# Kernel tuning notes

Measured on AMD Instinct MI355X. Metric: run time of the kernel, lower is better.

## Reference

```python
import jax, jax.numpy as jnp
import numpy as np


def _pair_loss(s, r):
    # s: [N, 4] sampled lidar, r: [M, 4] raw lidar; use xyz only
    a = s[:, :3]
    b = r[:, :3]
    # pairwise Euclidean distances, [N, M] (torch.cdist p=2)
    sq = (jnp.sum(a * a, axis=1)[:, None]
          + jnp.sum(b * b, axis=1)[None, :]
          - 2.0 * (a @ b.T))
    dist = jnp.sqrt(jnp.maximum(sq, 0.0))
    # dist[argmin(dim=0), j] == min over rows; dist[i, argmin(dim=1)] == min over cols
    min_over_sampled = jnp.min(dist, axis=0)  # [M] nearest sampled point per raw point
    min_over_raw = jnp.min(dist, axis=1)      # [N] nearest raw point per sampled point
    LB = jnp.mean(min_over_sampled)
    LF = jnp.mean(min_over_raw)
    LM = jnp.max(min_over_raw)
    return 5.0 * LB + 1.0 * LF + LM


def setup_inputs() -> dict:
    key = jax.random.key(0)
    k1, k2 = jax.random.split(key)
    B, N, M = 2, 4096, 16384
    sampled = jax.random.normal(k1, (B, N, 4), dtype=jnp.float32)
    raw = jax.random.normal(k2, (B, M, 4), dtype=jnp.float32)
    return {"sampled": sampled, "raw": raw}


def reference(sampled, raw):
    # list of pairs == batch dim; loss averaged over pairs
    losses = jax.vmap(_pair_loss)(sampled, raw)  # [B]
    return jnp.mean(losses)
```

## Files before the change

### kernel.cpp

```cpp
#include <hip/hip_runtime.h>
#include <math.h>

constexpr int BB = 2, NN = 4096, MM = 16384;
constexpr int CSL = 4;
constexpr int RSL = 16;
constexpr unsigned INFBITS = 0x7F800000u;
constexpr ushort ONEB = 0x3F80;

typedef __attribute__((ext_vector_type(8)))  short  short8;
typedef __attribute__((ext_vector_type(8)))  ushort ushort8;
typedef __attribute__((ext_vector_type(16))) float  f32x16;

__device__ __forceinline__ ushort f2bf(float f) {
    unsigned u = __float_as_uint(f);
    u += 0x7FFF + ((u >> 16) & 1);
    return (ushort)(u >> 16);
}
__device__ __forceinline__ void split2(float v, ushort& h, ushort& l) {
    h = f2bf(v);
    l = f2bf(v - __uint_as_float(((unsigned)h) << 16));
}
__device__ __forceinline__ float vmin16(const f32x16& c) {
    float a0 = fminf(fminf(c[0], c[1]),   fminf(c[2], c[3]));
    float a1 = fminf(fminf(c[4], c[5]),   fminf(c[6], c[7]));
    float a2 = fminf(fminf(c[8], c[9]),   fminf(c[10], c[11]));
    float a3 = fminf(fminf(c[12], c[13]), fminf(c[14], c[15]));
    return fminf(fminf(a0, a1), fminf(a2, a3));
}

__global__ __launch_bounds__(256) void pack_kernel(
    const float* __restrict__ sampled, const float* __restrict__ raw,
    ushort* __restrict__ As, ushort* __restrict__ Ar,
    unsigned* __restrict__ counter)
{
    const int g = blockIdx.x * 256 + threadIdx.x;
    if (g == 0) *counter = 0u;
    float4 v;
    ushort* dst;
    if (g < BB * NN) {
        v = ((const float4*)sampled)[g];
        dst = As + ((size_t)(g >> 5) << 9) + (g & 31) * 8;
    } else {
        const int p = g - BB * NN;
        v = ((const float4*)raw)[p];
        dst = Ar + ((size_t)(p >> 5) << 9) + (p & 31) * 8;
    }
    float n = fmaf(v.z, v.z, fmaf(v.y, v.y, v.x * v.x));
    ushort hx,lx,hy,ly,hz,lz,hn,ln;
    split2(-2.f * v.x, hx, lx); split2(-2.f * v.y, hy, ly);
    split2(-2.f * v.z, hz, lz); split2(n, hn, ln);
    *(ushort8*)(dst)       = ushort8{hx,hy,hz,hx,hy,hz,lx,ly};
    *(ushort8*)(dst + 256) = ushort8{lz,hn,ln,ONEB,ONEB,0,0,0};
}

__global__ __launch_bounds__(256) void pair_kernel(
    const float* __restrict__ sampled,
    const float* __restrict__ raw,
    const ushort* __restrict__ As, const ushort* __restrict__ Ar,
    float* __restrict__ rowpart,
    float* __restrict__ colpart)
{
    const int gx = blockIdx.x, tid = threadIdx.x;
    const int w = tid >> 6, lane = tid & 63, half = lane >> 5, l31 = lane & 31;
    const float INF = __uint_as_float(INFBITS);
    const f32x16 zero = {0.f,0.f,0.f,0.f,0.f,0.f,0.f,0.f,
                         0.f,0.f,0.f,0.f,0.f,0.f,0.f,0.f};

    int b, base, sl;
    const ushort* Ap;
    float4 v;
    float* outp;
    if (gx < 1024) {
        int idx = gx; b = idx >> 9; idx &= 511;
        const int og = idx >> 2; sl = idx & 3;
        base = og * 128 + w * 32;
        v = ((const float4*)raw)[(size_t)b * MM + base + l31];
        Ap = As + ((size_t)(b * (NN / 32) + sl * 32) << 9) + lane * 8;
        outp = colpart + ((size_t)sl * BB + b) * MM + base;
    } else {
        int idx = gx - 1024; b = idx >> 9; idx &= 511;
        const int og = idx >> 4; sl = idx & 15;
        base = og * 128 + w * 32;
        v = ((const float4*)sampled)[(size_t)b * NN + base + l31];
        Ap = Ar + ((size_t)(b * (MM / 32) + sl * 32) << 9) + lane * 8;
        outp = rowpart + ((size_t)sl * BB + b) * NN + base;
    }

    short8 bfr;
    {
        float n = fmaf(v.z, v.z, fmaf(v.y, v.y, v.x * v.x));
        ushort hx,lx,hy,ly,hz,lz,hn,ln;
        split2(v.x, hx, lx); split2(v.y, hy, ly);
        split2(v.z, hz, lz); split2(n, hn, ln);
        ushort8 w0 = ushort8{hx,hy,hz,lx,ly,lz,hx,hy};
        ushort8 w1 = ushort8{hz,ONEB,ONEB,hn,ln,0,0,0};
        ushort8 sel = half ? w1 : w0;
        bfr = *(short8*)&sel;
    }

    float acc = INF;
#pragma unroll 2
    for (int t = 0; t < 32; ++t) {
        short8 af = *(const short8*)(Ap + ((size_t)t << 9));
        f32x16 c = __builtin_amdgcn_mfma_f32_32x32x16_bf16(af, bfr, zero, 0, 0, 0);
        acc = fminf(acc, vmin16(c));
    }
    acc = fminf(acc, __shfl_xor(acc, 32, 64));
    if (lane < 32) outp[lane] = fmaxf(acc, 0.f);
}

__global__ __launch_bounds__(256) void reduce_kernel(
    const float* __restrict__ rowpart,
    const float* __restrict__ colpart,
    float* __restrict__ part,
    unsigned* __restrict__ counter,
    float* __restrict__ out)
{
    const int k = blockIdx.x, b = k >> 6, s = k & 63;
    const int tid = threadIdx.x;
    const float INF = __uint_as_float(INFBITS);

    const int col = s * 256 + tid;
    float v = INF;
#pragma unroll
    for (int sl = 0; sl < CSL; ++sl)
        v = fminf(v, colpart[((size_t)sl * BB + b) * MM + col]);
    float sB = sqrtf(v);

    const int row = s * 64 + (tid & 63);
    const int jq  = tid >> 6;
    float wv2 = INF;
#pragma unroll
    for (int q = 0; q < RSL / 4; ++q)
        wv2 = fminf(wv2, rowpart[((size_t)(jq * (RSL / 4) + q) * BB + b) * NN + row]);
    __shared__ float rred[4][64];
    rred[jq][tid & 63] = wv2;
    __syncthreads();
    float sF = 0.f, mF = 0.f;
    if (tid < 64) {
        float rmn = fminf(fminf(rred[0][tid], rred[1][tid]),
                          fminf(rred[2][tid], rred[3][tid]));
        float d = sqrtf(rmn);
        sF = d; mF = d;
    }

    for (int m = 1; m < 64; m <<= 1) {
        sB += __shfl_xor(sB, m, 64);
        sF += __shfl_xor(sF, m, 64);
        mF = fmaxf(mF, __shfl_xor(mF, m, 64));
    }
    __shared__ float red[3][4];
    const int lane = tid & 63, wvi = tid >> 6;
    if (lane == 0) { red[0][wvi] = sB; red[1][wvi] = sF; red[2][wvi] = mF; }
    __syncthreads();

    __shared__ bool isLast;
    if (tid == 0) {
        part[k * 3 + 0] = red[0][0] + red[0][1] + red[0][2] + red[0][3];
        part[k * 3 + 1] = red[1][0] + red[1][1] + red[1][2] + red[1][3];
        part[k * 3 + 2] = fmaxf(fmaxf(red[2][0], red[2][1]),
                                fmaxf(red[2][2], red[2][3]));
        __threadfence();
        isLast = (atomicAdd(counter, 1u) == 127u);
    }
    __syncthreads();
    if (!isLast) return;

    __threadfence();
    volatile const float* vp = part;
    float fB = 0.f, fF = 0.f, fM = 0.f;
    if (tid < 128) {
        fB = vp[tid * 3 + 0]; fF = vp[tid * 3 + 1]; fM = vp[tid * 3 + 2];
    }
    for (int m = 1; m < 64; m <<= 1) {
        fB += __shfl_xor(fB, m, 64);
        fF += __shfl_xor(fF, m, 64);
        fM = fmaxf(fM, __shfl_xor(fM, m, 64));
    }
    __shared__ float fin[2][3];
    if (tid < 128 && (tid & 63) == 0) {
        fin[tid >> 6][0] = fB; fin[tid >> 6][1] = fF; fin[tid >> 6][2] = fM;
    }
    __syncthreads();
    if (tid == 0) {
        float l0 = 5.f * fin[0][0] / (float)MM + fin[0][1] / (float)NN + fin[0][2];
        float l1 = 5.f * fin[1][0] / (float)MM + fin[1][1] / (float)NN + fin[1][2];
        *out = 0.5f * (l0 + l1);
    }
}

extern "C" void kernel_launch(void* const* d_in, const int* in_sizes, int n_in,
                              void* d_out, int out_size, void* d_ws, size_t ws_size,
                              hipStream_t stream) {
    const float* sampled = (const float*)d_in[0];
    const float* raw     = (const float*)d_in[1];
    ushort* As     = (ushort*)d_ws;
    ushort* Ar     = As + (size_t)BB * NN * 16;
    float* colpart = (float*)(Ar + (size_t)BB * MM * 16);
    float* rowpart = colpart + (size_t)CSL * BB * MM;
    float* part    = rowpart + (size_t)RSL * BB * NN;
    unsigned* counter = (unsigned*)(part + 3 * 128);
    float* out     = (float*)d_out;

    pack_kernel<<<(BB * (NN + MM)) / 256, 256, 0, stream>>>(sampled, raw, As, Ar, counter);
    pair_kernel<<<2048, 256, 0, stream>>>(sampled, raw, As, Ar, rowpart, colpart);
    reduce_kernel<<<128, 256, 0, stream>>>(rowpart, colpart, part, counter, out);
}
```

Baseline: 34.43 us.

## Register-block four point fragments per wave to reuse each A-fragment load

```diff
diff --git a/kernel.cpp b/kernel.cpp
--- a/kernel.cpp
+++ b/kernel.cpp
@@ -2,8 +2,8 @@
 #include <math.h>
 
 constexpr int BB = 2, NN = 4096, MM = 16384;
-constexpr int CSL = 4;
-constexpr int RSL = 16;
+constexpr int CSL = 8;
+constexpr int RSL = 32;
 constexpr unsigned INFBITS = 0x7F800000u;
 constexpr ushort ONEB = 0x3F80;
 
@@ -26,6 +26,16 @@
     float a2 = fminf(fminf(c[8], c[9]),   fminf(c[10], c[11]));
     float a3 = fminf(fminf(c[12], c[13]), fminf(c[14], c[15]));
     return fminf(fminf(a0, a1), fminf(a2, a3));
+}
+__device__ __forceinline__ short8 bfrag(float4 v, int half) {
+    float n = fmaf(v.z, v.z, fmaf(v.y, v.y, v.x * v.x));
+    ushort hx,lx,hy,ly,hz,lz,hn,ln;
+    split2(v.x, hx, lx); split2(v.y, hy, ly);
+    split2(v.z, hz, lz); split2(n, hn, ln);
+    ushort8 w0 = ushort8{hx,hy,hz,lx,ly,lz,hx,hy};
+    ushort8 w1 = ushort8{hz,ONEB,ONEB,hn,ln,0,0,0};
+    ushort8 sel = half ? w1 : w0;
+    return *(short8*)&sel;
 }
 
 __global__ __launch_bounds__(256) void pack_kernel(
@@ -53,7 +63,7 @@
     *(ushort8*)(dst + 256) = ushort8{lz,hn,ln,ONEB,ONEB,0,0,0};
 }
 
-__global__ __launch_bounds__(256) void pair_kernel(
+__global__ __launch_bounds__(256, 4) void pair_kernel(
     const float* __restrict__ sampled,
     const float* __restrict__ raw,
     const ushort* __restrict__ As, const ushort* __restrict__ Ar,
@@ -66,47 +76,54 @@
     const f32x16 zero = {0.f,0.f,0.f,0.f,0.f,0.f,0.f,0.f,
                          0.f,0.f,0.f,0.f,0.f,0.f,0.f,0.f};
 
-    int b, base, sl;
+    int b;
     const ushort* Ap;
-    float4 v;
+    const float4* ownp;
     float* outp;
-    if (gx < 1024) {
-        int idx = gx; b = idx >> 9; idx &= 511;
-        const int og = idx >> 2; sl = idx & 3;
-        base = og * 128 + w * 32;
-        v = ((const float4*)raw)[(size_t)b * MM + base + l31];
-        Ap = As + ((size_t)(b * (NN / 32) + sl * 32) << 9) + lane * 8;
-        outp = colpart + ((size_t)sl * BB + b) * MM + base;
+    if (gx < 512) {
+        int idx = gx; b = idx >> 8; idx &= 255;
+        const int ob = idx & 31, sl = idx >> 5;
+        const int own0 = ob * 512 + w * 128;
+        ownp = (const float4*)raw + (size_t)b * MM + own0 + l31;
+        Ap = As + (((size_t)(b * (NN / 32) + sl * 16)) << 9) + lane * 8;
+        outp = colpart + ((size_t)sl * BB + b) * MM + own0;
     } else {
-        int idx = gx - 1024; b = idx >> 9; idx &= 511;
-        const int og = idx >> 4; sl = idx & 15;
-        base = og * 128 + w * 32;
-        v = ((const float4*)sampled)[(size_t)b * NN + base + l31];
-        Ap = Ar + ((size_t)(b * (MM / 32) + sl * 32) << 9) + lane * 8;
-        outp = rowpart + ((size_t)sl * BB + b) * NN + base;
-    }
-
-    short8 bfr;
-    {
-        float n = fmaf(v.z, v.z, fmaf(v.y, v.y, v.x * v.x));
-        ushort hx,lx,hy,ly,hz,lz,hn,ln;
-        split2(v.x, hx, lx); split2(v.y, hy, ly);
-        split2(v.z, hz, lz); split2(n, hn, ln);
-        ushort8 w0 = ushort8{hx,hy,hz,lx,ly,lz,hx,hy};
-        ushort8 w1 = ushort8{hz,ONEB,ONEB,hn,ln,0,0,0};
-        ushort8 sel = half ? w1 : w0;
-        bfr = *(short8*)&sel;
-    }
-
-    float acc = INF;
-#pragma unroll 2
-    for (int t = 0; t < 32; ++t) {
+        int idx = gx - 512; b = idx >> 8; idx &= 255;
+        const int ob = idx & 7, sl = idx >> 3;
+        const int own0 = ob * 512 + w * 128;
+        ownp = (const float4*)sampled + (size_t)b * NN + own0 + l31;
+        Ap = Ar + (((size_t)(b * (MM / 32) + sl * 16)) << 9) + lane * 8;
+        outp = rowpart + ((size_t)sl * BB + b) * NN + own0;
+    }
+
+    short8 bfr0 = bfrag(ownp[0],  half);
+    short8 bfr1 = bfrag(ownp[32], half);
+    short8 bfr2 = bfrag(ownp[64], half);
+    short8 bfr3 = bfrag(ownp[96], half);
+
+    float acc0 = INF, acc1 = INF, acc2 = INF, acc3 = INF;
+#pragma unroll 1
+    for (int t = 0; t < 16; ++t) {
         short8 af = *(const short8*)(Ap + ((size_t)t << 9));
-        f32x16 c = __builtin_amdgcn_mfma_f32_32x32x16_bf16(af, bfr, zero, 0, 0, 0);
-        acc = fminf(acc, vmin16(c));
-    }
-    acc = fminf(acc, __shfl_xor(acc, 32, 64));
-    if (lane < 32) outp[lane] = fmaxf(acc, 0.f);
+        f32x16 c0 = __builtin_amdgcn_mfma_f32_32x32x16_bf16(af, bfr0, zero, 0, 0, 0);
+        acc0 = fminf(acc0, vmin16(c0));
+        f32x16 c1 = __builtin_amdgcn_mfma_f32_32x32x16_bf16(af, bfr1, zero, 0, 0, 0);
+        acc1 = fminf(acc1, vmin16(c1));
+        f32x16 c2 = __builtin_amdgcn_mfma_f32_32x32x16_bf16(af, bfr2, zero, 0, 0, 0);
+        acc2 = fminf(acc2, vmin16(c2));
+        f32x16 c3 = __builtin_amdgcn_mfma_f32_32x32x16_bf16(af, bfr3, zero, 0, 0, 0);
+        acc3 = fminf(acc3, vmin16(c3));
+    }
+    acc0 = fminf(acc0, __shfl_xor(acc0, 32, 64));
+    acc1 = fminf(acc1, __shfl_xor(acc1, 32, 64));
+    acc2 = fminf(acc2, __shfl_xor(acc2, 32, 64));
+    acc3 = fminf(acc3, __shfl_xor(acc3, 32, 64));
+    if (lane < 32) {
+        outp[lane]      = fmaxf(acc0, 0.f);
+        outp[32 + lane] = fmaxf(acc1, 0.f);
+        outp[64 + lane] = fmaxf(acc2, 0.f);
+        outp[96 + lane] = fmaxf(acc3, 0.f);
+    }
 }
 
 __global__ __launch_bounds__(256) void reduce_kernel(
@@ -203,6 +220,6 @@
     float* out     = (float*)d_out;
 
     pack_kernel<<<(BB * (NN + MM)) / 256, 256, 0, stream>>>(sampled, raw, As, Ar, counter);
-    pair_kernel<<<2048, 256, 0, stream>>>(sampled, raw, As, Ar, rowpart, colpart);
+    pair_kernel<<<1024, 256, 0, stream>>>(sampled, raw, As, Ar, rowpart, colpart);
     reduce_kernel<<<128, 256, 0, stream>>>(rowpart, colpart, part, counter, out);
 }
```

Result: no change. 34.45 us (+0.0%).
